# Kernel optimization log

Hardware: AMD Instinct MI355X
Metric: run time of the kernel (lower is better)

## Reference

```python
import jax, jax.numpy as jnp
import numpy as np

B, L, D, DFF = 4, 4096, 1024, 4096
EPS = 1e-6

def _rmsnorm(x, w):
    return x * jax.lax.rsqrt(jnp.mean(x * x, axis=-1, keepdims=True) + EPS) * w

def setup_inputs() -> dict:
    key = jax.random.key(0)
    ks = jax.random.split(key, 16)
    s = 1.0 / np.sqrt(D)
    sf = 1.0 / np.sqrt(DFF)
    return {
        "x": jax.random.normal(ks[0], (B, L, D), jnp.float32),
        # QuasiLSTM gate linears, stored [in, out]; y = x @ W + b
        "w_forget": jax.random.normal(ks[1], (D, D), jnp.float32) * s,
        "b_forget": jnp.zeros((D,), jnp.float32),
        "w_input": jax.random.normal(ks[2], (D, D), jnp.float32) * s,
        "b_input": jnp.zeros((D,), jnp.float32),
        "w_igate": jax.random.normal(ks[3], (D, D), jnp.float32) * s,
        "b_igate": jnp.zeros((D,), jnp.float32),
        "w_ogate": jax.random.normal(ks[4], (D, D), jnp.float32) * s,
        "b_ogate": jnp.zeros((D,), jnp.float32),
        "h0": jax.random.normal(ks[5], (D,), jnp.float32),  # last_hidden_init
        "norm1_w": jnp.ones((D,), jnp.float32),
        "norm2_w": jnp.ones((D,), jnp.float32),
        # FFN SwiGLU
        "w_fc": jax.random.normal(ks[6], (D, DFF), jnp.float32) * s,
        "b_fc": jnp.zeros((DFF,), jnp.float32),
        "w_fc_act": jax.random.normal(ks[7], (D, DFF), jnp.float32) * s,
        "b_fc_act": jnp.zeros((DFF,), jnp.float32),
        "w_out": jax.random.normal(ks[8], (DFF, D), jnp.float32) * sf,
        "b_out": jnp.zeros((D,), jnp.float32),
    }

def reference(x, w_forget, b_forget, w_input, b_input, w_igate, b_igate,
              w_ogate, b_ogate, h0, norm1_w, norm2_w,
              w_fc, b_fc, w_fc_act, b_fc_act, w_out, b_out):
    # --- QuasiLSTM branch (pre-norm residual) ---
    x_res = x
    xn = _rmsnorm(x, norm1_w)                                   # [B,L,D]
    forget = jax.nn.sigmoid(xn @ w_forget + b_forget)           # a_t
    inp = jnp.tanh(xn @ w_input + b_input) * jax.nn.sigmoid(xn @ w_igate + b_igate)  # b_t
    # Linear recurrence h_t = a_t * h_{t-1} + b_t, h_0 = 0 (inner chunk),
    # computed as an associative scan over the length axis.
    def comb(left, right):
        a_l, b_l = left
        a_r, b_r = right
        return (a_l * a_r, b_l * a_r + b_r)
    _, h_inner = jax.lax.associative_scan(comb, (forget, inp), axis=1)
    # cross-chunk contribution from last_hidden_init
    h = h_inner + h0[None, None, :] * jnp.cumprod(forget, axis=1)
    y = jnp.tanh(h) * jax.nn.sigmoid(xn @ w_ogate + b_ogate)
    x1 = y + x_res  # dropout p=0 -> identity
    # --- FFN SwiGLU branch ---
    xn2 = _rmsnorm(x1, norm2_w)
    hff = (xn2 @ w_fc + b_fc) * jax.nn.silu(xn2 @ w_fc_act + b_fc_act)
    out = hff @ w_out + b_out
    return out + x1
```

## Files before the change

### kernel.cpp

```cpp
#include <hip/hip_runtime.h>
#include <math.h>
#include <stdint.h>

static constexpr int Bb  = 4;
static constexpr int Ll  = 4096;
static constexpr int Dd  = 1024;
static constexpr int DFF = 4096;
static constexpr int Mm  = Bb * Ll;
static constexpr int CH  = 64;
static constexpr int CS  = Ll / CH;
static constexpr float EPS = 1e-6f;

typedef __attribute__((ext_vector_type(8))) short short8;
typedef __attribute__((ext_vector_type(4))) float floatx4;
typedef __attribute__((ext_vector_type(4))) unsigned short us4;

__device__ __forceinline__ float sigmoidf_(float v) { return 1.0f / (1.0f + __expf(-v)); }
__device__ __forceinline__ float fast_tanh(float x) {
    return 2.0f / (1.0f + __expf(-2.0f * x)) - 1.0f;
}
__device__ __forceinline__ ushort f2bf(float f) {
    union { float f; uint32_t u; } v; v.f = f;
    return (ushort)((v.u + 0x7FFFu + ((v.u >> 16) & 1u)) >> 16);
}
__device__ __forceinline__ float bf2f(ushort h) {
    union { uint32_t u; float f; } v; v.u = (uint32_t)h << 16; return v.f;
}

__device__ __forceinline__ void gload16(const ushort* g, ushort* l) {
    __builtin_amdgcn_global_load_lds(
        (const __attribute__((address_space(1))) uint32_t*)g,
        (__attribute__((address_space(3))) uint32_t*)l, 16, 0, 0);
}

__device__ __forceinline__ void stage128x32(const ushort* __restrict__ src, int ld,
                                            int r0, int k0, ushort* lds, int tid)
{
    #pragma unroll
    for (int h = 0; h < 2; ++h) {
        int c  = tid + h * 256;
        int m  = c >> 2;
        int kb = (c & 3) ^ ((m >> 1) & 3);
        gload16(src + (size_t)(r0 + m) * ld + k0 + kb * 8, lds + c * 8);
    }
}

__global__ __launch_bounds__(256, 2) void mfma_gemm_gates(
    const ushort* __restrict__ A, const ushort* __restrict__ W1t,
    const ushort* __restrict__ W2t,
    const float* __restrict__ b_input, const float* __restrict__ b_forget,
    const float* __restrict__ b_igate, const float* __restrict__ b_ogate,
    ushort* __restrict__ Ga, ushort* __restrict__ Gb, ushort* __restrict__ Gog,
    int K)
{
    __shared__ ushort As[128 * 32];
    __shared__ ushort B1s[128 * 32];
    __shared__ ushort B2s[128 * 32];
    int tid = threadIdx.x;
    int m0 = blockIdx.y * 128, n0 = blockIdx.x * 128;
    int wave = tid >> 6, lane = tid & 63;
    int wm = (wave >> 1) * 64, wn = (wave & 1) * 64;
    int fr = lane & 15, q = lane >> 4;
    int sw = (q ^ ((fr >> 1) & 3)) * 8;

    floatx4 acc1[4][4] = {};
    floatx4 acc2[4][4] = {};

    for (int k0 = 0; k0 < K; k0 += 32) {
        stage128x32(A,   K, m0, k0, As,  tid);
        stage128x32(W1t, K, n0, k0, B1s, tid);
        stage128x32(W2t, K, n0, k0, B2s, tid);
        __syncthreads();
        short8 a[4], b[4], c[4];
        #pragma unroll
        for (int mi = 0; mi < 4; ++mi)
            a[mi] = *(const short8*)&As[(wm + mi * 16 + fr) * 32 + sw];
        #pragma unroll
        for (int ni = 0; ni < 4; ++ni) {
            b[ni] = *(const short8*)&B1s[(wn + ni * 16 + fr) * 32 + sw];
            c[ni] = *(const short8*)&B2s[(wn + ni * 16 + fr) * 32 + sw];
        }
        #pragma unroll
        for (int mi = 0; mi < 4; ++mi)
            #pragma unroll
            for (int ni = 0; ni < 4; ++ni) {
                acc1[mi][ni] = __builtin_amdgcn_mfma_f32_16x16x32_bf16(
                    a[mi], b[ni], acc1[mi][ni], 0, 0, 0);
                acc2[mi][ni] = __builtin_amdgcn_mfma_f32_16x16x32_bf16(
                    a[mi], c[ni], acc2[mi][ni], 0, 0, 0);
            }
        __syncthreads();
    }

    #pragma unroll
    for (int ni = 0; ni < 4; ++ni) {
        int col = n0 + wn + ni * 16 + fr;
        if (col < 1024) {
            float b1v = b_input[col], b2v = b_igate[col];
            #pragma unroll
            for (int mi = 0; mi < 4; ++mi)
                #pragma unroll
                for (int r = 0; r < 4; ++r) {
                    int row = m0 + wm + mi * 16 + q * 4 + r;
                    float z1 = acc1[mi][ni][r] + b1v;
                    float z2 = acc2[mi][ni][r] + b2v;
                    Gb[(size_t)row * Dd + col] = f2bf(fast_tanh(z1) * sigmoidf_(z2));
                }
        } else {
            int c2 = col - 1024;
            float b1v = b_forget[c2], b2v = b_ogate[c2];
            #pragma unroll
            for (int mi = 0; mi < 4; ++mi)
                #pragma unroll
                for (int r = 0; r < 4; ++r) {
                    int row = m0 + wm + mi * 16 + q * 4 + r;
                    float z1 = acc1[mi][ni][r] + b1v;
                    float z2 = acc2[mi][ni][r] + b2v;
                    Ga[(size_t)row * Dd + c2]  = f2bf(sigmoidf_(z1));
                    Gog[(size_t)row * Dd + c2] = f2bf(sigmoidf_(z2));
                }
        }
    }
}

__global__ __launch_bounds__(256, 2) void mfma_gemm_swiglu(
    const ushort* __restrict__ A, const ushort* __restrict__ W1t,
    const float* __restrict__ b1, const ushort* __restrict__ W2t,
    const float* __restrict__ b2, ushort* __restrict__ C,
    int K, int ldC)
{
    __shared__ ushort As[128 * 32];
    __shared__ ushort B1s[128 * 32];
    __shared__ ushort B2s[128 * 32];
    int tid = threadIdx.x;
    int m0 = blockIdx.y * 128, n0 = blockIdx.x * 128;
    int wave = tid >> 6, lane = tid & 63;
    int wm = (wave >> 1) * 64, wn = (wave & 1) * 64;
    int fr = lane & 15, q = lane >> 4;
    int sw = (q ^ ((fr >> 1) & 3)) * 8;

    floatx4 acc1[4][4] = {};
    floatx4 acc2[4][4] = {};

    for (int k0 = 0; k0 < K; k0 += 32) {
        stage128x32(A,   K, m0, k0, As,  tid);
        stage128x32(W1t, K, n0, k0, B1s, tid);
        stage128x32(W2t, K, n0, k0, B2s, tid);
        __syncthreads();
        short8 a[4], b[4], c[4];
        #pragma unroll
        for (int mi = 0; mi < 4; ++mi)
            a[mi] = *(const short8*)&As[(wm + mi * 16 + fr) * 32 + sw];
        #pragma unroll
        for (int ni = 0; ni < 4; ++ni) {
            b[ni] = *(const short8*)&B1s[(wn + ni * 16 + fr) * 32 + sw];
            c[ni] = *(const short8*)&B2s[(wn + ni * 16 + fr) * 32 + sw];
        }
        #pragma unroll
        for (int mi = 0; mi < 4; ++mi)
            #pragma unroll
            for (int ni = 0; ni < 4; ++ni) {
                acc1[mi][ni] = __builtin_amdgcn_mfma_f32_16x16x32_bf16(
                    a[mi], b[ni], acc1[mi][ni], 0, 0, 0);
                acc2[mi][ni] = __builtin_amdgcn_mfma_f32_16x16x32_bf16(
                    a[mi], c[ni], acc2[mi][ni], 0, 0, 0);
            }
        __syncthreads();
    }

    #pragma unroll
    for (int ni = 0; ni < 4; ++ni) {
        int col = n0 + wn + ni * 16 + fr;
        float b1v = b1[col], b2v = b2[col];
        #pragma unroll
        for (int mi = 0; mi < 4; ++mi)
            #pragma unroll
            for (int r = 0; r < 4; ++r) {
                int row = m0 + wm + mi * 16 + q * 4 + r;
                float z1 = acc1[mi][ni][r] + b1v;
                float z2 = acc2[mi][ni][r] + b2v;
                C[(size_t)row * ldC + col] = f2bf(z1 * z2 * sigmoidf_(z2));
            }
    }
}

__global__ __launch_bounds__(256, 2) void mfma_gemm_residual(
    const ushort* __restrict__ A, const ushort* __restrict__ Wt,
    const float* __restrict__ bias, float* __restrict__ C,
    int K, int ldC)
{
    __shared__ ushort As[128 * 32];
    __shared__ ushort Bs[128 * 32];
    int tid = threadIdx.x;
    int m0 = blockIdx.y * 128, n0 = blockIdx.x * 128;
    int wave = tid >> 6, lane = tid & 63;
    int wm = (wave >> 1) * 64, wn = (wave & 1) * 64;
    int fr = lane & 15, q = lane >> 4;
    int sw = (q ^ ((fr >> 1) & 3)) * 8;

    floatx4 acc[4][4] = {};

    for (int k0 = 0; k0 < K; k0 += 32) {
        stage128x32(A,  K, m0, k0, As, tid);
        stage128x32(Wt, K, n0, k0, Bs, tid);
        __syncthreads();
        short8 a[4], b[4];
        #pragma unroll
        for (int mi = 0; mi < 4; ++mi)
            a[mi] = *(const short8*)&As[(wm + mi * 16 + fr) * 32 + sw];
        #pragma unroll
        for (int ni = 0; ni < 4; ++ni)
            b[ni] = *(const short8*)&Bs[(wn + ni * 16 + fr) * 32 + sw];
        #pragma unroll
        for (int mi = 0; mi < 4; ++mi)
            #pragma unroll
            for (int ni = 0; ni < 4; ++ni)
                acc[mi][ni] = __builtin_amdgcn_mfma_f32_16x16x32_bf16(
                    a[mi], b[ni], acc[mi][ni], 0, 0, 0);
        __syncthreads();
    }

    #pragma unroll
    for (int ni = 0; ni < 4; ++ni) {
        int col = n0 + wn + ni * 16 + fr;
        float bsv = bias[col];
        #pragma unroll
        for (int mi = 0; mi < 4; ++mi)
            #pragma unroll
            for (int r = 0; r < 4; ++r) {
                int row = m0 + wm + mi * 16 + q * 4 + r;
                size_t idx = (size_t)row * ldC + col;
                C[idx] = acc[mi][ni][r] + bsv + C[idx];
            }
    }
}

__global__ __launch_bounds__(256) void transpose_cast_kernel(
    const float* __restrict__ W, ushort* __restrict__ Wt, int K, int N)
{
    __shared__ float t[32][33];
    int lx = threadIdx.x & 31, ly = threadIdx.x >> 5;
    int n = blockIdx.x * 32 + lx;
    #pragma unroll
    for (int i = 0; i < 4; ++i) {
        int k = blockIdx.y * 32 + ly + i * 8;
        t[ly + i * 8][lx] = W[(size_t)k * N + n];
    }
    __syncthreads();
    int k2 = blockIdx.y * 32 + lx;
    #pragma unroll
    for (int i = 0; i < 4; ++i) {
        int n2 = blockIdx.x * 32 + ly + i * 8;
        Wt[(size_t)n2 * K + k2] = f2bf(t[lx][ly + i * 8]);
    }
}

__global__ __launch_bounds__(256) void transpose_cast_gates(
    const float* __restrict__ w_i, const float* __restrict__ w_f,
    const float* __restrict__ w_g, const float* __restrict__ w_o,
    ushort* __restrict__ W1t, ushort* __restrict__ W2t)
{
    int z = blockIdx.z;
    const float* W = (z == 0) ? w_i : (z == 1) ? w_f : (z == 2) ? w_g : w_o;
    ushort* Wt = (z == 0) ? W1t : (z == 1) ? W1t + (size_t)1024 * Dd
               : (z == 2) ? W2t : W2t + (size_t)1024 * Dd;
    __shared__ float t[32][33];
    int lx = threadIdx.x & 31, ly = threadIdx.x >> 5;
    int n = blockIdx.x * 32 + lx;
    #pragma unroll
    for (int i = 0; i < 4; ++i) {
        int k = blockIdx.y * 32 + ly + i * 8;
        t[ly + i * 8][lx] = W[(size_t)k * Dd + n];
    }
    __syncthreads();
    int k2 = blockIdx.y * 32 + lx;
    #pragma unroll
    for (int i = 0; i < 4; ++i) {
        int n2 = blockIdx.x * 32 + ly + i * 8;
        Wt[(size_t)n2 * Dd + k2] = f2bf(t[lx][ly + i * 8]);
    }
}

__global__ __launch_bounds__(256) void rmsnorm_bf16_kernel(
    const float* __restrict__ x, const float* __restrict__ w,
    ushort* __restrict__ o)
{
    int row = blockIdx.x;
    int tid = threadIdx.x;
    float4 v = ((const float4*)(x + (size_t)row * Dd))[tid];
    float ss = v.x*v.x + v.y*v.y + v.z*v.z + v.w*v.w;
    #pragma unroll
    for (int off = 32; off > 0; off >>= 1) ss += __shfl_down(ss, off, 64);
    __shared__ float red[4];
    if ((tid & 63) == 0) red[tid >> 6] = ss;
    __syncthreads();
    float scale = rsqrtf((red[0] + red[1] + red[2] + red[3]) * (1.0f / Dd) + EPS);
    float4 wv = ((const float4*)w)[tid];
    us4 ov;
    ov.x = f2bf(v.x * scale * wv.x);
    ov.y = f2bf(v.y * scale * wv.y);
    ov.z = f2bf(v.z * scale * wv.z);
    ov.w = f2bf(v.w * scale * wv.w);
    *(us4*)&o[(size_t)row * Dd + tid * 4] = ov;
}

__global__ __launch_bounds__(256) void scan_pass1(
    const ushort* __restrict__ Ga, const ushort* __restrict__ Gb,
    float* __restrict__ P, float* __restrict__ Hend)
{
    int tid = threadIdx.x;
    int c = blockIdx.x, b = blockIdx.y;
    size_t base = ((size_t)b * Ll + (size_t)c * CS) * Dd + tid * 4;
    float p[4] = {1.f, 1.f, 1.f, 1.f};
    float h[4] = {};
    #pragma unroll 4
    for (int t = 0; t < CS; ++t) {
        us4 av = *(const us4*)&Ga[base + (size_t)t * Dd];
        us4 bv = *(const us4*)&Gb[base + (size_t)t * Dd];
        #pragma unroll
        for (int j = 0; j < 4; ++j) {
            float aa = bf2f(av[j]);
            float bb = bf2f(bv[j]);
            p[j] *= aa;
            h[j] = aa * h[j] + bb;
        }
    }
    size_t o = ((size_t)b * CH + c) * Dd + tid * 4;
    *(float4*)&P[o]    = make_float4(p[0], p[1], p[2], p[3]);
    *(float4*)&Hend[o] = make_float4(h[0], h[1], h[2], h[3]);
}

__global__ __launch_bounds__(256) void scan_pass2(
    const float* __restrict__ P, const float* __restrict__ Hend,
    const float* __restrict__ h0, float* __restrict__ Carry)
{
    int idx = blockIdx.x * 256 + threadIdx.x;
    int b = idx / Dd, d = idx % Dd;
    float carry = h0[d];
    for (int c = 0; c < CH; ++c) {
        size_t o = ((size_t)b * CH + c) * Dd + d;
        Carry[o] = carry;
        carry = P[o] * carry + Hend[o];
    }
}

__global__ __launch_bounds__(256) void scan_pass3_norm(
    const ushort* __restrict__ Ga, const ushort* __restrict__ Gb,
    const ushort* __restrict__ Gog, const float* __restrict__ Carry,
    const float* __restrict__ x, const float* __restrict__ norm2w,
    float* __restrict__ x1, ushort* __restrict__ xnb)
{
    int tid = threadIdx.x;
    int c = blockIdx.x, b = blockIdx.y;
    size_t base = ((size_t)b * Ll + (size_t)c * CS) * Dd + tid * 4;
    float4 h4 = *(const float4*)&Carry[((size_t)b * CH + c) * Dd + tid * 4];
    float h[4] = {h4.x, h4.y, h4.z, h4.w};
    float4 w4 = ((const float4*)norm2w)[tid];
    float wv[4] = {w4.x, w4.y, w4.z, w4.w};
    __shared__ float red[4];

    for (int t = 0; t < CS; ++t) {
        size_t i = base + (size_t)t * Dd;
        us4 av = *(const us4*)&Ga[i];
        us4 bv = *(const us4*)&Gb[i];
        us4 gv = *(const us4*)&Gog[i];
        float4 xv = *(const float4*)&x[i];
        float xs[4] = {xv.x, xv.y, xv.z, xv.w};
        float v[4];
        #pragma unroll
        for (int j = 0; j < 4; ++j) {
            float aa = bf2f(av[j]);
            float bb = bf2f(bv[j]);
            h[j] = aa * h[j] + bb;
            v[j] = fast_tanh(h[j]) * bf2f(gv[j]) + xs[j];
        }
        *(float4*)&x1[i] = make_float4(v[0], v[1], v[2], v[3]);
        float ss = v[0]*v[0] + v[1]*v[1] + v[2]*v[2] + v[3]*v[3];
        #pragma unroll
        for (int off = 32; off > 0; off >>= 1) ss += __shfl_down(ss, off, 64);
        if ((tid & 63) == 0) red[tid >> 6] = ss;
        __syncthreads();
        float scale = rsqrtf((red[0] + red[1] + red[2] + red[3]) * (1.0f / Dd) + EPS);
        us4 ov;
        #pragma unroll
        for (int j = 0; j < 4; ++j) ov[j] = f2bf(v[j] * scale * wv[j]);
        *(us4*)&xnb[i] = ov;
        __syncthreads();
    }
}

extern "C" void kernel_launch(void* const* d_in, const int* in_sizes, int n_in,
                              void* d_out, int out_size, void* d_ws, size_t ws_size,
                              hipStream_t stream)
{
    const float* x        = (const float*)d_in[0];
    const float* w_forget = (const float*)d_in[1];
    const float* b_forget = (const float*)d_in[2];
    const float* w_input  = (const float*)d_in[3];
    const float* b_input  = (const float*)d_in[4];
    const float* w_igate  = (const float*)d_in[5];
    const float* b_igate  = (const float*)d_in[6];
    const float* w_ogate  = (const float*)d_in[7];
    const float* b_ogate  = (const float*)d_in[8];
    const float* h0       = (const float*)d_in[9];
    const float* norm1_w  = (const float*)d_in[10];
    const float* norm2_w  = (const float*)d_in[11];
    const float* w_fc     = (const float*)d_in[12];
    const float* b_fc     = (const float*)d_in[13];
    const float* w_fc_act = (const float*)d_in[14];
    const float* b_fc_act = (const float*)d_in[15];
    const float* w_out    = (const float*)d_in[16];
    const float* b_out    = (const float*)d_in[17];
    float* out = (float*)d_out;

    char* ws = (char*)d_ws;
    const size_t MB = 1ull << 20;
    ushort* wtG1  = (ushort*)(ws + 0 * MB);
    ushort* wtG2  = (ushort*)(ws + 4 * MB);
    ushort* wtFC  = (ushort*)(ws + 8 * MB);
    ushort* wtFCA = (ushort*)(ws + 16 * MB);
    ushort* wtOUT = (ushort*)(ws + 24 * MB);
    ushort* xnb   = (ushort*)(ws + 32 * MB);
    ushort* Ga    = (ushort*)(ws + 64 * MB);
    ushort* Gb    = (ushort*)(ws + 96 * MB);
    ushort* Gog   = (ushort*)(ws + 128 * MB);
    ushort* hff   = (ushort*)(ws + 64 * MB);
    float*  P     = (float*)(ws + 192 * MB);
    float*  Hend  = (float*)(ws + 193 * MB);
    float*  Carry = (float*)(ws + 194 * MB);

    transpose_cast_gates<<<dim3(32, 32, 4), 256, 0, stream>>>(
        w_input, w_forget, w_igate, w_ogate, wtG1, wtG2);
    transpose_cast_kernel<<<dim3(DFF/32, Dd/32), 256, 0, stream>>>(w_fc,     wtFC,  Dd, DFF);
    transpose_cast_kernel<<<dim3(DFF/32, Dd/32), 256, 0, stream>>>(w_fc_act, wtFCA, Dd, DFF);
    transpose_cast_kernel<<<dim3(Dd/32, DFF/32), 256, 0, stream>>>(w_out,    wtOUT, DFF, Dd);

    rmsnorm_bf16_kernel<<<Mm, 256, 0, stream>>>(x, norm1_w, xnb);

    dim3 gg(2048 / 128, Mm / 128);
    mfma_gemm_gates<<<gg, 256, 0, stream>>>(xnb, wtG1, wtG2,
                                            b_input, b_forget, b_igate, b_ogate,
                                            Ga, Gb, Gog, Dd);

    dim3 sg(CH, Bb);
    scan_pass1<<<sg, 256, 0, stream>>>(Ga, Gb, P, Hend);
    scan_pass2<<<(Bb * Dd) / 256, 256, 0, stream>>>(P, Hend, h0, Carry);
    scan_pass3_norm<<<sg, 256, 0, stream>>>(Ga, Gb, Gog, Carry, x, norm2_w,
                                            out, xnb);

    dim3 gf(DFF / 128, Mm / 128);
    mfma_gemm_swiglu<<<gf, 256, 0, stream>>>(xnb, wtFC, b_fc, wtFCA, b_fc_act,
                                             hff, Dd, DFF);

    dim3 go(Dd / 128, Mm / 128);
    mfma_gemm_residual<<<go, 256, 0, stream>>>(hff, wtOUT, b_out, out, DFF, Dd);
}
```

Measured before the change: 994.7 us.

## Rewrite MFMA GEMMs as 256x256 tiles with triple-buffered async LDS pipeline

```diff
diff --git a/kernel.cpp b/kernel.cpp
--- a/kernel.cpp
+++ b/kernel.cpp
@@ -33,75 +33,128 @@
         (__attribute__((address_space(3))) uint32_t*)l, 16, 0, 0);
 }
 
-__device__ __forceinline__ void stage128x32(const ushort* __restrict__ src, int ld,
-                                            int r0, int k0, ushort* lds, int tid)
-{
-    #pragma unroll
-    for (int h = 0; h < 2; ++h) {
-        int c  = tid + h * 256;
-        int m  = c >> 2;
-        int kb = (c & 3) ^ ((m >> 1) & 3);
-        gload16(src + (size_t)(r0 + m) * ld + k0 + kb * 8, lds + c * 8);
-    }
-}
-
-__global__ __launch_bounds__(256, 2) void mfma_gemm_gates(
-    const ushort* __restrict__ A, const ushort* __restrict__ W1t,
-    const ushort* __restrict__ W2t,
-    const float* __restrict__ b_input, const float* __restrict__ b_forget,
-    const float* __restrict__ b_igate, const float* __restrict__ b_ogate,
-    ushort* __restrict__ Ga, ushort* __restrict__ Gb, ushort* __restrict__ Gog,
-    int K)
-{
-    __shared__ ushort As[128 * 32];
-    __shared__ ushort B1s[128 * 32];
-    __shared__ ushort B2s[128 * 32];
-    int tid = threadIdx.x;
-    int m0 = blockIdx.y * 128, n0 = blockIdx.x * 128;
-    int wave = tid >> 6, lane = tid & 63;
-    int wm = (wave >> 1) * 64, wn = (wave & 1) * 64;
-    int fr = lane & 15, q = lane >> 4;
-    int sw = (q ^ ((fr >> 1) & 3)) * 8;
-
-    floatx4 acc1[4][4] = {};
-    floatx4 acc2[4][4] = {};
-
-    for (int k0 = 0; k0 < K; k0 += 32) {
-        stage128x32(A,   K, m0, k0, As,  tid);
-        stage128x32(W1t, K, n0, k0, B1s, tid);
-        stage128x32(W2t, K, n0, k0, B2s, tid);
-        __syncthreads();
-        short8 a[4], b[4], c[4];
-        #pragma unroll
-        for (int mi = 0; mi < 4; ++mi)
-            a[mi] = *(const short8*)&As[(wm + mi * 16 + fr) * 32 + sw];
-        #pragma unroll
-        for (int ni = 0; ni < 4; ++ni) {
-            b[ni] = *(const short8*)&B1s[(wn + ni * 16 + fr) * 32 + sw];
-            c[ni] = *(const short8*)&B2s[(wn + ni * 16 + fr) * 32 + sw];
-        }
-        #pragma unroll
-        for (int mi = 0; mi < 4; ++mi)
+static constexpr int TILE_US = 256 * 32;
+static constexpr int BUF_US  = 2 * TILE_US;
+
+__device__ __forceinline__ void gemm_core_512(
+    const ushort* __restrict__ A, const ushort* __restrict__ B1,
+    const ushort* __restrict__ B2, int m0, int n0b1, int n0b2, int K,
+    ushort* lds, floatx4 (&acc1)[8][2], floatx4 (&acc2)[8][2])
+{
+    const int tid = threadIdx.x;
+    const int cm = tid >> 2;
+    const int kb = (tid & 3) ^ ((cm >> 1) & 3);
+    const ushort* pa0 = A  + (size_t)(m0 + cm) * K + kb * 8;
+    const ushort* pa1 = pa0 + (size_t)128 * K;
+    const ushort* pb0 = B1 + (size_t)(n0b1 + cm) * K + kb * 8;
+    const ushort* pb1 = B2 + (size_t)(n0b2 + cm) * K + kb * 8;
+
+    const int wave = tid >> 6, lane = tid & 63;
+    const int wr = wave >> 2, wc = wave & 3;
+    const int fr = lane & 15, q = lane >> 4;
+
+    int offA[8], offB[2], offC[2];
+    #pragma unroll
+    for (int mi = 0; mi < 8; ++mi) {
+        int r = wr * 128 + mi * 16 + fr;
+        offA[mi] = r * 32 + ((q ^ ((r >> 1) & 3)) << 3);
+    }
+    #pragma unroll
+    for (int ni = 0; ni < 2; ++ni) {
+        int r1 = wc * 32 + ni * 16 + fr;
+        offB[ni] = r1 * 32 + ((q ^ ((r1 >> 1) & 3)) << 3);
+        int r2 = r1 + 128;
+        offC[ni] = r2 * 32 + ((q ^ ((r2 >> 1) & 3)) << 3);
+    }
+
+    const int NT = K >> 5;
+
+    {
+        ushort* As0 = lds;
+        ushort* Bs0 = lds + TILE_US;
+        gload16(pa0, As0 + tid * 8); gload16(pa1, As0 + (tid + 512) * 8);
+        gload16(pb0, Bs0 + tid * 8); gload16(pb1, Bs0 + (tid + 512) * 8);
+        pa0 += 32; pa1 += 32; pb0 += 32; pb1 += 32;
+        ushort* As1 = lds + BUF_US;
+        ushort* Bs1 = As1 + TILE_US;
+        gload16(pa0, As1 + tid * 8); gload16(pa1, As1 + (tid + 512) * 8);
+        gload16(pb0, Bs1 + tid * 8); gload16(pb1, Bs1 + (tid + 512) * 8);
+        pa0 += 32; pa1 += 32; pb0 += 32; pb1 += 32;
+        asm volatile("s_waitcnt vmcnt(4)" ::: "memory");
+        __builtin_amdgcn_s_barrier();
+    }
+
+    int cur = 0;
+    for (int t = 0; t < NT; ++t) {
+        if (t + 2 < NT) {
+            int nxt2 = cur + 2; if (nxt2 >= 3) nxt2 -= 3;
+            ushort* As2 = lds + nxt2 * BUF_US;
+            ushort* Bs2 = As2 + TILE_US;
+            gload16(pa0, As2 + tid * 8); gload16(pa1, As2 + (tid + 512) * 8);
+            gload16(pb0, Bs2 + tid * 8); gload16(pb1, Bs2 + (tid + 512) * 8);
+            pa0 += 32; pa1 += 32; pb0 += 32; pb1 += 32;
+        }
+        const ushort* As = lds + cur * BUF_US;
+        const ushort* Bs = As + TILE_US;
+        short8 a[8], b[2], c[2];
+        #pragma unroll
+        for (int mi = 0; mi < 8; ++mi) a[mi] = *(const short8*)&As[offA[mi]];
+        #pragma unroll
+        for (int ni = 0; ni < 2; ++ni) {
+            b[ni] = *(const short8*)&Bs[offB[ni]];
+            c[ni] = *(const short8*)&Bs[offC[ni]];
+        }
+        __builtin_amdgcn_s_setprio(1);
+        #pragma unroll
+        for (int mi = 0; mi < 8; ++mi)
             #pragma unroll
-            for (int ni = 0; ni < 4; ++ni) {
+            for (int ni = 0; ni < 2; ++ni) {
                 acc1[mi][ni] = __builtin_amdgcn_mfma_f32_16x16x32_bf16(
                     a[mi], b[ni], acc1[mi][ni], 0, 0, 0);
                 acc2[mi][ni] = __builtin_amdgcn_mfma_f32_16x16x32_bf16(
                     a[mi], c[ni], acc2[mi][ni], 0, 0, 0);
             }
-        __syncthreads();
-    }
-
-    #pragma unroll
-    for (int ni = 0; ni < 4; ++ni) {
-        int col = n0 + wn + ni * 16 + fr;
+        __builtin_amdgcn_s_setprio(0);
+        if (t + 2 < NT) {
+            asm volatile("s_waitcnt vmcnt(4) lgkmcnt(0)" ::: "memory");
+        } else {
+            asm volatile("s_waitcnt vmcnt(0) lgkmcnt(0)" ::: "memory");
+        }
+        __builtin_amdgcn_s_barrier();
+        cur = (cur + 1 == 3) ? 0 : cur + 1;
+    }
+}
+
+__global__ __launch_bounds__(512) void mfma_gemm_gates(
+    const ushort* __restrict__ A, const ushort* __restrict__ W1t,
+    const ushort* __restrict__ W2t,
+    const float* __restrict__ b_input, const float* __restrict__ b_forget,
+    const float* __restrict__ b_igate, const float* __restrict__ b_ogate,
+    ushort* __restrict__ Ga, ushort* __restrict__ Gb, ushort* __restrict__ Gog)
+{
+    __shared__ __align__(16) ushort lds[3 * BUF_US];
+    constexpr int GXN = 2048 / 128;
+    const int nwg = (2048 / 128) * (Mm / 256);
+    int s = (blockIdx.x & 7) * (nwg >> 3) + (blockIdx.x >> 3);
+    int bx = s % GXN, by = s / GXN;
+    int m0 = by * 256, n0 = bx * 128;
+
+    floatx4 acc1[8][2] = {};
+    floatx4 acc2[8][2] = {};
+    gemm_core_512(A, W1t, W2t, m0, n0, n0, Dd, lds, acc1, acc2);
+
+    int tid = threadIdx.x, wave = tid >> 6, lane = tid & 63;
+    int wr = wave >> 2, wc = wave & 3, fr = lane & 15, q = lane >> 4;
+    #pragma unroll
+    for (int ni = 0; ni < 2; ++ni) {
+        int col = n0 + wc * 32 + ni * 16 + fr;
         if (col < 1024) {
             float b1v = b_input[col], b2v = b_igate[col];
             #pragma unroll
-            for (int mi = 0; mi < 4; ++mi)
+            for (int mi = 0; mi < 8; ++mi)
                 #pragma unroll
                 for (int r = 0; r < 4; ++r) {
-                    int row = m0 + wm + mi * 16 + q * 4 + r;
+                    int row = m0 + wr * 128 + mi * 16 + q * 4 + r;
                     float z1 = acc1[mi][ni][r] + b1v;
                     float z2 = acc2[mi][ni][r] + b2v;
                     Gb[(size_t)row * Dd + col] = f2bf(fast_tanh(z1) * sigmoidf_(z2));
@@ -110,10 +163,10 @@
             int c2 = col - 1024;
             float b1v = b_forget[c2], b2v = b_ogate[c2];
             #pragma unroll
-            for (int mi = 0; mi < 4; ++mi)
+            for (int mi = 0; mi < 8; ++mi)
                 #pragma unroll
                 for (int r = 0; r < 4; ++r) {
-                    int row = m0 + wm + mi * 16 + q * 4 + r;
+                    int row = m0 + wr * 128 + mi * 16 + q * 4 + r;
                     float z1 = acc1[mi][ni][r] + b1v;
                     float z2 = acc2[mi][ni][r] + b2v;
                     Ga[(size_t)row * Dd + c2]  = f2bf(sigmoidf_(z1));
@@ -123,114 +176,71 @@
     }
 }
 
-__global__ __launch_bounds__(256, 2) void mfma_gemm_swiglu(
+__global__ __launch_bounds__(512) void mfma_gemm_swiglu(
     const ushort* __restrict__ A, const ushort* __restrict__ W1t,
     const float* __restrict__ b1, const ushort* __restrict__ W2t,
-    const float* __restrict__ b2, ushort* __restrict__ C,
-    int K, int ldC)
-{
-    __shared__ ushort As[128 * 32];
-    __shared__ ushort B1s[128 * 32];
-    __shared__ ushort B2s[128 * 32];
-    int tid = threadIdx.x;
-    int m0 = blockIdx.y * 128, n0 = blockIdx.x * 128;
-    int wave = tid >> 6, lane = tid & 63;
-    int wm = (wave >> 1) * 64, wn = (wave & 1) * 64;
-    int fr = lane & 15, q = lane >> 4;
-    int sw = (q ^ ((fr >> 1) & 3)) * 8;
-
-    floatx4 acc1[4][4] = {};
-    floatx4 acc2[4][4] = {};
-
-    for (int k0 = 0; k0 < K; k0 += 32) {
-        stage128x32(A,   K, m0, k0, As,  tid);
-        stage128x32(W1t, K, n0, k0, B1s, tid);
-        stage128x32(W2t, K, n0, k0, B2s, tid);
-        __syncthreads();
-        short8 a[4], b[4], c[4];
-        #pragma unroll
-        for (int mi = 0; mi < 4; ++mi)
-            a[mi] = *(const short8*)&As[(wm + mi * 16 + fr) * 32 + sw];
-        #pragma unroll
-        for (int ni = 0; ni < 4; ++ni) {
-            b[ni] = *(const short8*)&B1s[(wn + ni * 16 + fr) * 32 + sw];
-            c[ni] = *(const short8*)&B2s[(wn + ni * 16 + fr) * 32 + sw];
-        }
-        #pragma unroll
-        for (int mi = 0; mi < 4; ++mi)
-            #pragma unroll
-            for (int ni = 0; ni < 4; ++ni) {
-                acc1[mi][ni] = __builtin_amdgcn_mfma_f32_16x16x32_bf16(
-                    a[mi], b[ni], acc1[mi][ni], 0, 0, 0);
-                acc2[mi][ni] = __builtin_amdgcn_mfma_f32_16x16x32_bf16(
-                    a[mi], c[ni], acc2[mi][ni], 0, 0, 0);
-            }
-        __syncthreads();
-    }
-
-    #pragma unroll
-    for (int ni = 0; ni < 4; ++ni) {
-        int col = n0 + wn + ni * 16 + fr;
+    const float* __restrict__ b2, ushort* __restrict__ C)
+{
+    __shared__ __align__(16) ushort lds[3 * BUF_US];
+    constexpr int GXN = DFF / 128;
+    const int nwg = (DFF / 128) * (Mm / 256);
+    int s = (blockIdx.x & 7) * (nwg >> 3) + (blockIdx.x >> 3);
+    int bx = s % GXN, by = s / GXN;
+    int m0 = by * 256, n0 = bx * 128;
+
+    floatx4 acc1[8][2] = {};
+    floatx4 acc2[8][2] = {};
+    gemm_core_512(A, W1t, W2t, m0, n0, n0, Dd, lds, acc1, acc2);
+
+    int tid = threadIdx.x, wave = tid >> 6, lane = tid & 63;
+    int wr = wave >> 2, wc = wave & 3, fr = lane & 15, q = lane >> 4;
+    #pragma unroll
+    for (int ni = 0; ni < 2; ++ni) {
+        int col = n0 + wc * 32 + ni * 16 + fr;
         float b1v = b1[col], b2v = b2[col];
         #pragma unroll
-        for (int mi = 0; mi < 4; ++mi)
+        for (int mi = 0; mi < 8; ++mi)
             #pragma unroll
             for (int r = 0; r < 4; ++r) {
-                int row = m0 + wm + mi * 16 + q * 4 + r;
+                int row = m0 + wr * 128 + mi * 16 + q * 4 + r;
                 float z1 = acc1[mi][ni][r] + b1v;
                 float z2 = acc2[mi][ni][r] + b2v;
-                C[(size_t)row * ldC + col] = f2bf(z1 * z2 * sigmoidf_(z2));
+                C[(size_t)row * DFF + col] = f2bf(z1 * z2 * sigmoidf_(z2));
             }
     }
 }
 
-__global__ __launch_bounds__(256, 2) void mfma_gemm_residual(
+__global__ __launch_bounds__(512) void mfma_gemm_residual(
     const ushort* __restrict__ A, const ushort* __restrict__ Wt,
-    const float* __restrict__ bias, float* __restrict__ C,
-    int K, int ldC)
-{
-    __shared__ ushort As[128 * 32];
-    __shared__ ushort Bs[128 * 32];
-    int tid = threadIdx.x;
-    int m0 = blockIdx.y * 128, n0 = blockIdx.x * 128;
-    int wave = tid >> 6, lane = tid & 63;
-    int wm = (wave >> 1) * 64, wn = (wave & 1) * 64;
-    int fr = lane & 15, q = lane >> 4;
-    int sw = (q ^ ((fr >> 1) & 3)) * 8;
-
-    floatx4 acc[4][4] = {};
-
-    for (int k0 = 0; k0 < K; k0 += 32) {
-        stage128x32(A,  K, m0, k0, As, tid);
-        stage128x32(Wt, K, n0, k0, Bs, tid);
-        __syncthreads();
-        short8 a[4], b[4];
-        #pragma unroll
-        for (int mi = 0; mi < 4; ++mi)
-            a[mi] = *(const short8*)&As[(wm + mi * 16 + fr) * 32 + sw];
-        #pragma unroll
-        for (int ni = 0; ni < 4; ++ni)
-            b[ni] = *(const short8*)&Bs[(wn + ni * 16 + fr) * 32 + sw];
-        #pragma unroll
-        for (int mi = 0; mi < 4; ++mi)
-            #pragma unroll
-            for (int ni = 0; ni < 4; ++ni)
-                acc[mi][ni] = __builtin_amdgcn_mfma_f32_16x16x32_bf16(
-                    a[mi], b[ni], acc[mi][ni], 0, 0, 0);
-        __syncthreads();
-    }
-
-    #pragma unroll
-    for (int ni = 0; ni < 4; ++ni) {
-        int col = n0 + wn + ni * 16 + fr;
-        float bsv = bias[col];
-        #pragma unroll
-        for (int mi = 0; mi < 4; ++mi)
+    const float* __restrict__ bias, float* __restrict__ C)
+{
+    __shared__ __align__(16) ushort lds[3 * BUF_US];
+    constexpr int GXN = Dd / 256;
+    const int nwg = (Dd / 256) * (Mm / 256);
+    int s = (blockIdx.x & 7) * (nwg >> 3) + (blockIdx.x >> 3);
+    int bx = s % GXN, by = s / GXN;
+    int m0 = by * 256, n0 = bx * 256;
+
+    floatx4 acc1[8][2] = {};
+    floatx4 acc2[8][2] = {};
+    gemm_core_512(A, Wt, Wt, m0, n0, n0 + 128, DFF, lds, acc1, acc2);
+
+    int tid = threadIdx.x, wave = tid >> 6, lane = tid & 63;
+    int wr = wave >> 2, wc = wave & 3, fr = lane & 15, q = lane >> 4;
+    #pragma unroll
+    for (int ni = 0; ni < 2; ++ni) {
+        int col1 = n0 + wc * 32 + ni * 16 + fr;
+        int col2 = col1 + 128;
+        float bs1 = bias[col1], bs2 = bias[col2];
+        #pragma unroll
+        for (int mi = 0; mi < 8; ++mi)
             #pragma unroll
             for (int r = 0; r < 4; ++r) {
-                int row = m0 + wm + mi * 16 + q * 4 + r;
-                size_t idx = (size_t)row * ldC + col;
-                C[idx] = acc[mi][ni][r] + bsv + C[idx];
+                int row = m0 + wr * 128 + mi * 16 + q * 4 + r;
+                size_t i1 = (size_t)row * Dd + col1;
+                size_t i2 = (size_t)row * Dd + col2;
+                C[i1] = acc1[mi][ni][r] + bs1 + C[i1];
+                C[i2] = acc2[mi][ni][r] + bs2 + C[i2];
             }
     }
 }
@@ -437,10 +447,8 @@
 
     rmsnorm_bf16_kernel<<<Mm, 256, 0, stream>>>(x, norm1_w, xnb);
 
-    dim3 gg(2048 / 128, Mm / 128);
-    mfma_gemm_gates<<<gg, 256, 0, stream>>>(xnb, wtG1, wtG2,
-                                            b_input, b_forget, b_igate, b_ogate,
-                                            Ga, Gb, Gog, Dd);
+    mfma_gemm_gates<<<(2048/128) * (Mm/256), 512, 0, stream>>>(
+        xnb, wtG1, wtG2, b_input, b_forget, b_igate, b_ogate, Ga, Gb, Gog);
 
     dim3 sg(CH, Bb);
     scan_pass1<<<sg, 256, 0, stream>>>(Ga, Gb, P, Hend);
@@ -448,10 +456,9 @@
     scan_pass3_norm<<<sg, 256, 0, stream>>>(Ga, Gb, Gog, Carry, x, norm2_w,
                                             out, xnb);
 
-    dim3 gf(DFF / 128, Mm / 128);
-    mfma_gemm_swiglu<<<gf, 256, 0, stream>>>(xnb, wtFC, b_fc, wtFCA, b_fc_act,
-                                             hff, Dd, DFF);
-
-    dim3 go(Dd / 128, Mm / 128);
-    mfma_gemm_residual<<<go, 256, 0, stream>>>(hff, wtOUT, b_out, out, DFF, Dd);
-}
+    mfma_gemm_swiglu<<<(DFF/128) * (Mm/256), 512, 0, stream>>>(
+        xnb, wtFC, b_fc, wtFCA, b_fc_act, hff);
+
+    mfma_gemm_residual<<<(Dd/256) * (Mm/256), 512, 0, stream>>>(
+        hff, wtOUT, b_out, out);
+}
```

Measured after the change: 869.6 us. 12.6% less time.
